# Optimization experiments

Hardware: AMD Instinct MI355X
Metric: run time of the kernel (lower is better)

## Reference

```python
import jax, jax.numpy as jnp
import numpy as np

EPS = 1e-5
SIGMA = 1.0

def _conv(x, w, stride):
    return jax.lax.conv_general_dilated(
        x, w, window_strides=(stride, stride),
        padding=[(w.shape[2] // 2, w.shape[2] // 2), (w.shape[3] // 2, w.shape[3] // 2)],
        dimension_numbers=('NCHW', 'OIHW', 'NCHW'))

def _bn(x, gamma, beta, mean, var):
    # inference-mode batchnorm over channel dim (NCHW)
    inv = gamma / jnp.sqrt(var + EPS)
    return x * inv[None, :, None, None] + (beta - mean * inv)[None, :, None, None]

def setup_inputs() -> dict:
    key = jax.random.key(0)
    ks = jax.random.split(key, 8)
    B, M, H, W, K = 8, 128, 64, 64, 6
    x = jax.random.normal(ks[0], (B, M, H, W), jnp.float32)
    cf = jax.random.normal(ks[1], (B, M, H, W), jnp.float32)
    w1 = jax.random.normal(ks[2], (M // 2, M, 3, 3), jnp.float32) * 0.05
    w2 = jax.random.normal(ks[3], (M // 4, M // 2, 3, 3), jnp.float32) * 0.05
    w3 = jax.random.normal(ks[4], (K, M // 4, 1, 1), jnp.float32) * 0.05
    def bn_params(k, c):
        k1, k2 = jax.random.split(k)
        return (jnp.ones((c,), jnp.float32),
                jnp.zeros((c,), jnp.float32),
                jax.random.normal(k1, (c,), jnp.float32) * 0.1,
                jnp.abs(jax.random.normal(k2, (c,), jnp.float32)) * 0.1 + 1.0)
    g1, b1, m1, v1 = bn_params(ks[5], M // 2)
    g2, b2, m2, v2 = bn_params(ks[6], M // 4)
    g3, b3, m3, v3 = bn_params(ks[7], K)
    return dict(x=x, center_features=cf, w1=w1, g1=g1, b1=b1, m1=m1, v1=v1,
                w2=w2, g2=g2, b2=b2, m2=m2, v2=v2,
                w3=w3, g3=g3, b3=b3, m3=m3, v3=v3)

def reference(x, center_features, w1, g1, b1, m1, v1, w2, g2, b2, m2, v2, w3, g3, b3, m3, v3):
    # center branch: conv-bn-relu x2 (stride 2) + 1x1 conv-bn, then spatial mean
    c = jax.nn.relu(_bn(_conv(center_features, w1, 2), g1, b1, m1, v1))
    c = jax.nn.relu(_bn(_conv(c, w2, 2), g2, b2, m2, v2))
    c = _bn(_conv(c, w3, 1), g3, b3, m3, v3)
    centers = c.reshape(c.shape[0], c.shape[1], -1).mean(axis=2)  # [B, K]

    B, C, H, W = x.shape
    K = centers.shape[-1]
    xf = x.reshape(B, C, H * W, 1)                      # [B,C,HW,1]
    cb = centers[:, None, None, :]                      # [B,1,1,K]
    dist = (xf - cb) ** 2                               # [B,C,HW,K]
    phi_soft = jax.nn.softmax(-SIGMA * dist, axis=-1)
    qsoft = jnp.sum(phi_soft * cb, axis=-1).reshape(B, C, H, W)
    symbols = jnp.argmin(dist, axis=-1)                 # [B,C,HW] (== argmax of hard softmax)
    qhard = centers[jnp.arange(B)[:, None, None], symbols].reshape(B, C, H, W)
    qbar = qsoft + jax.lax.stop_gradient(qhard - qsoft)
    return qbar, qsoft, qhard, symbols.reshape(B, C, H, W), centers
```

## Files before the change

### kernel.cpp

```cpp
#include <hip/hip_runtime.h>
#include <math.h>

#define BN_EPS 1e-5
#define SIGMA 1.0f

__global__ __launch_bounds__(256) void w1_to_f64_kernel(
    const float* __restrict__ w1, double* __restrict__ w1d)
{
    int i = blockIdx.x * 256 + threadIdx.x;
    if (i >= 73728) return;
    int j   = i & 7;
    int t   = i >> 3;
    int k   = t % 9;
    int t2  = t / 9;
    int ic  = t2 & 15;
    int t3  = t2 >> 4;
    int isp = t3 & 7;
    int ocg = t3 >> 3;
    w1d[i] = (double)w1[((ocg * 8 + j) * 128 + isp * 16 + ic) * 9 + k];
}

__global__ __launch_bounds__(256, 4) void conv1_partial_kernel(
    const float* __restrict__ in, const double* __restrict__ w1d,
    float* __restrict__ part)
{
    int bid = blockIdx.x;
    int oht = bid & 1;
    int b   = (bid >> 1) & 7;
    int isp = (bid >> 4) & 7;
    int ocg = bid >> 7;

    int tid = threadIdx.x;
    int ow  = tid & 31;
    int ohp = tid >> 5;
    int oh0 = oht * 16 + ohp * 2;
    int ih0 = 2 * oh0 - 1;
    int iw0 = 2 * ow - 1;

    const double* wb = w1d + (size_t)(ocg * 8 + isp) * 1152;

    double acc0[8], acc1[8];
    #pragma unroll
    for (int j = 0; j < 8; ++j) { acc0[j] = 0.0; acc1[j] = 0.0; }

    bool rowok[5], colok[3];
    #pragma unroll
    for (int t = 0; t < 5; ++t) rowok[t] = (ih0 + t) >= 0;
    #pragma unroll
    for (int t = 0; t < 3; ++t) colok[t] = (iw0 + t) >= 0;

    const float* base0 = in + ((size_t)(b * 128 + isp * 16) * 64 + ih0) * 64 + iw0;

    float cur[15];
    #pragma unroll
    for (int t = 0; t < 5; ++t)
        #pragma unroll
        for (int kw = 0; kw < 3; ++kw)
            cur[t * 3 + kw] = (rowok[t] && colok[kw]) ? base0[t * 64 + kw] : 0.f;

    for (int ic = 0; ic < 16; ++ic) {
        float nxt[15];
        if (ic + 1 < 16) {
            const float* basen = base0 + (size_t)(ic + 1) * 4096;
            #pragma unroll
            for (int t = 0; t < 5; ++t)
                #pragma unroll
                for (int kw = 0; kw < 3; ++kw)
                    nxt[t * 3 + kw] = (rowok[t] && colok[kw]) ? basen[t * 64 + kw] : 0.f;
        }
        double xv[15];
        #pragma unroll
        for (int i = 0; i < 15; ++i) xv[i] = (double)cur[i];

        const double* wk = wb + ic * 72;
        #pragma unroll
        for (int k = 0; k < 9; ++k) {
            int kh = k / 3, kw = k % 3;
            double2 wa = *(const double2*)&wk[k * 8 + 0];
            double2 wb2 = *(const double2*)&wk[k * 8 + 2];
            double2 wc = *(const double2*)&wk[k * 8 + 4];
            double2 wd = *(const double2*)&wk[k * 8 + 6];
            double x0 = xv[kh * 3 + kw];
            double x1 = xv[(kh + 2) * 3 + kw];
            acc0[0] = fma(x0, wa.x, acc0[0]);   acc1[0] = fma(x1, wa.x, acc1[0]);
            acc0[1] = fma(x0, wa.y, acc0[1]);   acc1[1] = fma(x1, wa.y, acc1[1]);
            acc0[2] = fma(x0, wb2.x, acc0[2]);  acc1[2] = fma(x1, wb2.x, acc1[2]);
            acc0[3] = fma(x0, wb2.y, acc0[3]);  acc1[3] = fma(x1, wb2.y, acc1[3]);
            acc0[4] = fma(x0, wc.x, acc0[4]);   acc1[4] = fma(x1, wc.x, acc1[4]);
            acc0[5] = fma(x0, wc.y, acc0[5]);   acc1[5] = fma(x1, wc.y, acc1[5]);
            acc0[6] = fma(x0, wd.x, acc0[6]);   acc1[6] = fma(x1, wd.x, acc1[6]);
            acc0[7] = fma(x0, wd.y, acc0[7]);   acc1[7] = fma(x1, wd.y, acc1[7]);
        }
        #pragma unroll
        for (int i = 0; i < 15; ++i) cur[i] = nxt[i];
    }

    #pragma unroll
    for (int j = 0; j < 8; ++j) {
        int idx0 = ((b * 64 + ocg * 8 + j) * 32 + oh0) * 32 + ow;
        part[isp * 524288 + idx0]      = (float)acc0[j];
        part[isp * 524288 + idx0 + 32] = (float)acc1[j];
    }
}

__global__ __launch_bounds__(256) void conv2_partial_kernel(
    const float* __restrict__ part1,
    const float* __restrict__ g1, const float* __restrict__ be1,
    const float* __restrict__ mn1, const float* __restrict__ vr1,
    const float* __restrict__ w,
    float* __restrict__ part)
{
    __shared__ float tin[4][33][36];
    __shared__ float twt[4][9][8];
    __shared__ double sinv[4], ssh[4];

    int bid = blockIdx.x;
    int ocg = bid & 3;
    int b   = (bid >> 2) & 7;
    int isp = bid >> 5;

    int tid = threadIdx.x;
    int ow  = tid & 15;
    int oh  = tid >> 4;

    if (tid < 4) {
        int ch = isp * 4 + tid;
        double inv = (double)g1[ch] / sqrt((double)vr1[ch] + BN_EPS);
        sinv[tid] = inv;
        ssh[tid]  = (double)be1[ch] - (double)mn1[ch] * inv;
    }
    __syncthreads();

    for (int lin = tid; lin < 4 * 33 * 34; lin += 256) {
        int c   = lin % 34;
        int t2  = lin / 34;
        int rr  = t2 % 33;
        int icc = t2 / 33;
        int ih  = rr - 1;
        int iw  = c - 1;
        float v = 0.f;
        if ((unsigned)ih < 32u && (unsigned)iw < 32u) {
            int ch  = isp * 4 + icc;
            int idx = ((b * 64 + ch) * 32 + ih) * 32 + iw;
            double s = 0.0;
            #pragma unroll
            for (int p = 0; p < 8; ++p) s += (double)part1[idx + p * 524288];
            double o = s * sinv[icc] + ssh[icc];
            v = fmaxf((float)o, 0.f);
        }
        tin[icc][rr][c] = v;
    }
    for (int i = tid; i < 288; i += 256) {
        int j   = i & 7;
        int k   = (i >> 3) % 9;
        int icc = i / 72;
        twt[icc][k][j] = w[(ocg * 8 + j) * 576 + (isp * 4 + icc) * 9 + k];
    }
    __syncthreads();

    double acc[8];
    #pragma unroll
    for (int j = 0; j < 8; ++j) acc[j] = 0.0;

    for (int icc = 0; icc < 4; ++icc) {
        double xv[9];
        #pragma unroll
        for (int kh = 0; kh < 3; ++kh)
            #pragma unroll
            for (int kw = 0; kw < 3; ++kw)
                xv[kh * 3 + kw] = (double)tin[icc][2 * oh + kh][2 * ow + kw];
        #pragma unroll
        for (int k = 0; k < 9; ++k) {
            float4 wa = *(const float4*)&twt[icc][k][0];
            float4 wb = *(const float4*)&twt[icc][k][4];
            acc[0] = fma(xv[k], (double)wa.x, acc[0]);
            acc[1] = fma(xv[k], (double)wa.y, acc[1]);
            acc[2] = fma(xv[k], (double)wa.z, acc[2]);
            acc[3] = fma(xv[k], (double)wa.w, acc[3]);
            acc[4] = fma(xv[k], (double)wb.x, acc[4]);
            acc[5] = fma(xv[k], (double)wb.y, acc[5]);
            acc[6] = fma(xv[k], (double)wb.z, acc[6]);
            acc[7] = fma(xv[k], (double)wb.w, acc[7]);
        }
    }
    int obase = ((b * 32 + ocg * 8) * 16 + oh) * 16 + ow;
    #pragma unroll
    for (int j = 0; j < 8; ++j)
        part[isp * 65536 + obase + j * 256] = (float)acc[j];
}

__global__ __launch_bounds__(256) void conv2_combine_ybar_kernel(
    const float* __restrict__ part,
    const float* __restrict__ g, const float* __restrict__ be,
    const float* __restrict__ mn, const float* __restrict__ vr,
    double* __restrict__ ybar)
{
    __shared__ double sm[4];
    int j  = blockIdx.x;
    int oc = j & 31;
    int t  = threadIdx.x;
    int idx = j * 256 + t;
    double s = 0.0;
    #pragma unroll
    for (int p = 0; p < 16; ++p) s += (double)part[idx + p * 65536];
    double inv = (double)g[oc] / sqrt((double)vr[oc] + BN_EPS);
    double o = s * inv + ((double)be[oc] - (double)mn[oc] * inv);
    double v = fmax(o, 0.0);
    #pragma unroll
    for (int off = 32; off > 0; off >>= 1) v += __shfl_down(v, off, 64);
    if ((t & 63) == 0) sm[t >> 6] = v;
    __syncthreads();
    if (t == 0) ybar[j] = (sm[0] + sm[1] + sm[2] + sm[3]) * (1.0 / 256.0);
}

__global__ __launch_bounds__(64) void centers_kernel(
    const double* __restrict__ ybar, const float* __restrict__ w3,
    const float* __restrict__ g, const float* __restrict__ be,
    const float* __restrict__ mn, const float* __restrict__ vr,
    double* __restrict__ cen_ws, float* __restrict__ cen_out)
{
    int t = threadIdx.x;
    if (t < 48) {
        int b = t / 6;
        int k = t % 6;
        double acc = 0.0;
        for (int ic = 0; ic < 32; ++ic) acc = fma((double)w3[k * 32 + ic], ybar[b * 32 + ic], acc);
        double inv = (double)g[k] / sqrt((double)vr[k] + BN_EPS);
        double c = acc * inv + ((double)be[k] - (double)mn[k] * inv);
        cen_ws[t]  = c;
        cen_out[t] = (float)c;
    }
}

__global__ __launch_bounds__(256) void quant_kernel(
    const float* __restrict__ x, const double* __restrict__ centers,
    float* __restrict__ qbar, float* __restrict__ qsoft,
    float* __restrict__ qhard, float* __restrict__ sym)
{
    int vid = blockIdx.x * 256 + threadIdx.x;
    int b = vid >> 17;

    double c[6];
    float cf[6];
    #pragma unroll
    for (int k = 0; k < 6; ++k) { c[k] = centers[b * 6 + k]; cf[k] = (float)c[k]; }

    float4 xv = ((const float4*)x)[vid];
    float xs[4] = {xv.x, xv.y, xv.z, xv.w};
    float r_bar[4], r_soft[4], r_hard[4], r_sym[4];

    #pragma unroll
    for (int i = 0; i < 4; ++i) {
        double xx = (double)xs[i];
        double d[6];
        double dmin = 1e300;
        int amin = 0;
        #pragma unroll
        for (int k = 0; k < 6; ++k) {
            double t = xx - c[k];
            d[k] = t * t;
            if (d[k] < dmin) { dmin = d[k]; amin = k; }
        }
        float se = 0.f, sw = 0.f;
        #pragma unroll
        for (int k = 0; k < 6; ++k) {
            float e = __expf(SIGMA * (float)(dmin - d[k]));
            se += e;
            sw += e * cf[k];
        }
        float qs = sw / se;
        float qh = cf[amin];
        r_soft[i] = qs;
        r_hard[i] = qh;
        r_bar[i]  = qh;
        r_sym[i]  = (float)amin;
    }

    ((float4*)qbar)[vid]  = make_float4(r_bar[0],  r_bar[1],  r_bar[2],  r_bar[3]);
    ((float4*)qsoft)[vid] = make_float4(r_soft[0], r_soft[1], r_soft[2], r_soft[3]);
    ((float4*)qhard)[vid] = make_float4(r_hard[0], r_hard[1], r_hard[2], r_hard[3]);
    ((float4*)sym)[vid]   = make_float4(r_sym[0],  r_sym[1],  r_sym[2],  r_sym[3]);
}

extern "C" void kernel_launch(void* const* d_in, const int* in_sizes, int n_in,
                              void* d_out, int out_size, void* d_ws, size_t ws_size,
                              hipStream_t stream) {
    const float* x  = (const float*)d_in[0];
    const float* cf = (const float*)d_in[1];
    const float* w1 = (const float*)d_in[2];
    const float* g1 = (const float*)d_in[3];
    const float* b1 = (const float*)d_in[4];
    const float* m1 = (const float*)d_in[5];
    const float* v1 = (const float*)d_in[6];
    const float* w2 = (const float*)d_in[7];
    const float* g2 = (const float*)d_in[8];
    const float* b2 = (const float*)d_in[9];
    const float* m2 = (const float*)d_in[10];
    const float* v2 = (const float*)d_in[11];
    const float* w3 = (const float*)d_in[12];
    const float* g3 = (const float*)d_in[13];
    const float* b3 = (const float*)d_in[14];
    const float* m3 = (const float*)d_in[15];
    const float* v3 = (const float*)d_in[16];

    const int NELEM = 8 * 128 * 64 * 64;
    float* out   = (float*)d_out;
    float* qbar  = out;
    float* qsoft = out + (size_t)NELEM;
    float* qhard = out + (size_t)2 * NELEM;
    float* sym   = out + (size_t)3 * NELEM;
    float* cen_o = out + (size_t)4 * NELEM;

    char* ws = (char*)d_ws;
    float*  part1 = (float*)(ws);
    float*  part2 = (float*)(ws + 16777216);
    double* yb    = (double*)(ws + 20971520);
    double* cen   = (double*)(ws + 20973568);
    double* w1d   = (double*)(ws + 20975616);

    w1_to_f64_kernel<<<288, 256, 0, stream>>>(w1, w1d);
    conv1_partial_kernel<<<1024, 256, 0, stream>>>(cf, w1d, part1);
    conv2_partial_kernel<<<512, 256, 0, stream>>>(part1, g1, b1, m1, v1, w2, part2);
    conv2_combine_ybar_kernel<<<256, 256, 0, stream>>>(part2, g2, b2, m2, v2, yb);
    centers_kernel<<<1, 64, 0, stream>>>(yb, w3, g3, b3, m3, v3, cen, cen_o);
    quant_kernel<<<NELEM / 4 / 256, 256, 0, stream>>>(x, cen, qbar, qsoft, qhard, sym);
}
```

Baseline: 188.0 us.

## Split conv1 input channels 16 ways and add separate combine+BN+ReLU kernel

Conv1's input-channel split becomes a template parameter. When the workspace is large enough it uses 16 splits, doubling the block count to 2048 for more parallelism. The partial-sum reduction, BN and ReLU move out of conv2's halo load into a dedicated vectorized combine kernel that writes y1 once. Previously each conv2 tile summed 8 partials per halo element, redundantly. The change adds an extra kernel launch and more partial-buffer traffic with 16 splits, and it drops the occupancy hint of 4 from conv1's launch bounds.

```diff
diff --git a/kernel.cpp b/kernel.cpp
--- a/kernel.cpp
+++ b/kernel.cpp
@@ -4,31 +4,35 @@
 #define BN_EPS 1e-5
 #define SIGMA 1.0f
 
+template<int NSPLIT>
 __global__ __launch_bounds__(256) void w1_to_f64_kernel(
     const float* __restrict__ w1, double* __restrict__ w1d)
 {
+    constexpr int ICN = 128 / NSPLIT;
     int i = blockIdx.x * 256 + threadIdx.x;
     if (i >= 73728) return;
     int j   = i & 7;
     int t   = i >> 3;
     int k   = t % 9;
     int t2  = t / 9;
-    int ic  = t2 & 15;
-    int t3  = t2 >> 4;
-    int isp = t3 & 7;
-    int ocg = t3 >> 3;
-    w1d[i] = (double)w1[((ocg * 8 + j) * 128 + isp * 16 + ic) * 9 + k];
-}
-
-__global__ __launch_bounds__(256, 4) void conv1_partial_kernel(
+    int ic  = t2 % ICN;
+    int t3  = t2 / ICN;
+    int isp = t3 % NSPLIT;
+    int ocg = t3 / NSPLIT;
+    w1d[i] = (double)w1[((ocg * 8 + j) * 128 + isp * ICN + ic) * 9 + k];
+}
+
+template<int NSPLIT>
+__global__ __launch_bounds__(256) void conv1_partial_kernel(
     const float* __restrict__ in, const double* __restrict__ w1d,
     float* __restrict__ part)
 {
+    constexpr int ICN = 128 / NSPLIT;
     int bid = blockIdx.x;
     int oht = bid & 1;
     int b   = (bid >> 1) & 7;
-    int isp = (bid >> 4) & 7;
-    int ocg = bid >> 7;
+    int isp = (bid >> 4) & (NSPLIT - 1);
+    int ocg = bid >> (NSPLIT == 8 ? 7 : 8);
 
     int tid = threadIdx.x;
     int ow  = tid & 31;
@@ -37,7 +41,7 @@
     int ih0 = 2 * oh0 - 1;
     int iw0 = 2 * ow - 1;
 
-    const double* wb = w1d + (size_t)(ocg * 8 + isp) * 1152;
+    const double* wb = w1d + ((size_t)ocg * NSPLIT + isp) * (ICN * 72);
 
     double acc0[8], acc1[8];
     #pragma unroll
@@ -49,7 +53,7 @@
     #pragma unroll
     for (int t = 0; t < 3; ++t) colok[t] = (iw0 + t) >= 0;
 
-    const float* base0 = in + ((size_t)(b * 128 + isp * 16) * 64 + ih0) * 64 + iw0;
+    const float* base0 = in + ((size_t)(b * 128 + isp * ICN) * 64 + ih0) * 64 + iw0;
 
     float cur[15];
     #pragma unroll
@@ -58,9 +62,9 @@
         for (int kw = 0; kw < 3; ++kw)
             cur[t * 3 + kw] = (rowok[t] && colok[kw]) ? base0[t * 64 + kw] : 0.f;
 
-    for (int ic = 0; ic < 16; ++ic) {
+    for (int ic = 0; ic < ICN; ++ic) {
         float nxt[15];
-        if (ic + 1 < 16) {
+        if (ic + 1 < ICN) {
             const float* basen = base0 + (size_t)(ic + 1) * 4096;
             #pragma unroll
             for (int t = 0; t < 5; ++t)
@@ -98,21 +102,43 @@
     #pragma unroll
     for (int j = 0; j < 8; ++j) {
         int idx0 = ((b * 64 + ocg * 8 + j) * 32 + oh0) * 32 + ow;
-        part[isp * 524288 + idx0]      = (float)acc0[j];
-        part[isp * 524288 + idx0 + 32] = (float)acc1[j];
-    }
+        part[(size_t)isp * 524288 + idx0]      = (float)acc0[j];
+        part[(size_t)isp * 524288 + idx0 + 32] = (float)acc1[j];
+    }
+}
+
+template<int NSPLIT>
+__global__ __launch_bounds__(256) void conv1_combine_kernel(
+    const float* __restrict__ part,
+    const float* __restrict__ g, const float* __restrict__ be,
+    const float* __restrict__ mn, const float* __restrict__ vr,
+    float* __restrict__ y1)
+{
+    int vid = blockIdx.x * 256 + threadIdx.x;
+    int idx = vid * 4;
+    int oc  = (idx >> 10) & 63;
+    double s0 = 0.0, s1 = 0.0, s2 = 0.0, s3 = 0.0;
+    #pragma unroll
+    for (int p = 0; p < NSPLIT; ++p) {
+        float4 v = *(const float4*)&part[idx + (size_t)p * 524288];
+        s0 += (double)v.x; s1 += (double)v.y; s2 += (double)v.z; s3 += (double)v.w;
+    }
+    double inv = (double)g[oc] / sqrt((double)vr[oc] + BN_EPS);
+    double sh  = (double)be[oc] - (double)mn[oc] * inv;
+    float4 o;
+    o.x = fmaxf((float)(s0 * inv + sh), 0.f);
+    o.y = fmaxf((float)(s1 * inv + sh), 0.f);
+    o.z = fmaxf((float)(s2 * inv + sh), 0.f);
+    o.w = fmaxf((float)(s3 * inv + sh), 0.f);
+    *(float4*)&y1[idx] = o;
 }
 
 __global__ __launch_bounds__(256) void conv2_partial_kernel(
-    const float* __restrict__ part1,
-    const float* __restrict__ g1, const float* __restrict__ be1,
-    const float* __restrict__ mn1, const float* __restrict__ vr1,
-    const float* __restrict__ w,
+    const float* __restrict__ y1, const float* __restrict__ w,
     float* __restrict__ part)
 {
     __shared__ float tin[4][33][36];
     __shared__ float twt[4][9][8];
-    __shared__ double sinv[4], ssh[4];
 
     int bid = blockIdx.x;
     int ocg = bid & 3;
@@ -123,13 +149,7 @@
     int ow  = tid & 15;
     int oh  = tid >> 4;
 
-    if (tid < 4) {
-        int ch = isp * 4 + tid;
-        double inv = (double)g1[ch] / sqrt((double)vr1[ch] + BN_EPS);
-        sinv[tid] = inv;
-        ssh[tid]  = (double)be1[ch] - (double)mn1[ch] * inv;
-    }
-    __syncthreads();
+    const float* inb = y1 + (size_t)(b * 64 + isp * 4) * 1024;
 
     for (int lin = tid; lin < 4 * 33 * 34; lin += 256) {
         int c   = lin % 34;
@@ -139,15 +159,8 @@
         int ih  = rr - 1;
         int iw  = c - 1;
         float v = 0.f;
-        if ((unsigned)ih < 32u && (unsigned)iw < 32u) {
-            int ch  = isp * 4 + icc;
-            int idx = ((b * 64 + ch) * 32 + ih) * 32 + iw;
-            double s = 0.0;
-            #pragma unroll
-            for (int p = 0; p < 8; ++p) s += (double)part1[idx + p * 524288];
-            double o = s * sinv[icc] + ssh[icc];
-            v = fmaxf((float)o, 0.f);
-        }
+        if ((unsigned)ih < 32u && (unsigned)iw < 32u)
+            v = inb[(icc * 32 + ih) * 32 + iw];
         tin[icc][rr][c] = v;
     }
     for (int i = tid; i < 288; i += 256) {
@@ -312,16 +325,41 @@
     float* cen_o = out + (size_t)4 * NELEM;
 
     char* ws = (char*)d_ws;
-    float*  part1 = (float*)(ws);
-    float*  part2 = (float*)(ws + 16777216);
-    double* yb    = (double*)(ws + 20971520);
-    double* cen   = (double*)(ws + 20973568);
-    double* w1d   = (double*)(ws + 20975616);
-
-    w1_to_f64_kernel<<<288, 256, 0, stream>>>(w1, w1d);
-    conv1_partial_kernel<<<1024, 256, 0, stream>>>(cf, w1d, part1);
-    conv2_partial_kernel<<<512, 256, 0, stream>>>(part1, g1, b1, m1, v1, w2, part2);
-    conv2_combine_ybar_kernel<<<256, 256, 0, stream>>>(part2, g2, b2, m2, v2, yb);
-    centers_kernel<<<1, 64, 0, stream>>>(yb, w3, g3, b3, m3, v3, cen, cen_o);
-    quant_kernel<<<NELEM / 4 / 256, 256, 0, stream>>>(x, cen, qbar, qsoft, qhard, sym);
-}
+    bool big = ws_size >= ((size_t)42 << 20);
+
+    if (big) {
+        const int NS = 16;
+        float*  part1 = (float*)(ws);
+        float*  y1    = (float*)(ws + (size_t)NS * 2097152);
+        float*  part2 = (float*)(ws + (size_t)NS * 2097152 + 2097152);
+        char*   tail  = ws + (size_t)NS * 2097152 + 2097152 + 4194304;
+        double* yb    = (double*)(tail);
+        double* cen   = (double*)(tail + 4096);
+        double* w1d   = (double*)(tail + 8192);
+
+        w1_to_f64_kernel<NS><<<288, 256, 0, stream>>>(w1, w1d);
+        conv1_partial_kernel<NS><<<2048, 256, 0, stream>>>(cf, w1d, part1);
+        conv1_combine_kernel<NS><<<512, 256, 0, stream>>>(part1, g1, b1, m1, v1, y1);
+        conv2_partial_kernel<<<512, 256, 0, stream>>>(y1, w2, part2);
+        conv2_combine_ybar_kernel<<<256, 256, 0, stream>>>(part2, g2, b2, m2, v2, yb);
+        centers_kernel<<<1, 64, 0, stream>>>(yb, w3, g3, b3, m3, v3, cen, cen_o);
+        quant_kernel<<<NELEM / 4 / 256, 256, 0, stream>>>(x, cen, qbar, qsoft, qhard, sym);
+    } else {
+        const int NS = 8;
+        float*  part1 = (float*)(ws);
+        float*  y1    = (float*)(ws + (size_t)NS * 2097152);
+        float*  part2 = (float*)(ws + (size_t)NS * 2097152 + 2097152);
+        char*   tail  = ws + (size_t)NS * 2097152 + 2097152 + 4194304;
+        double* yb    = (double*)(tail);
+        double* cen   = (double*)(tail + 4096);
+        double* w1d   = (double*)(tail + 8192);
+
+        w1_to_f64_kernel<NS><<<288, 256, 0, stream>>>(w1, w1d);
+        conv1_partial_kernel<NS><<<1024, 256, 0, stream>>>(cf, w1d, part1);
+        conv1_combine_kernel<NS><<<512, 256, 0, stream>>>(part1, g1, b1, m1, v1, y1);
+        conv2_partial_kernel<<<512, 256, 0, stream>>>(y1, w2, part2);
+        conv2_combine_ybar_kernel<<<256, 256, 0, stream>>>(part2, g2, b2, m2, v2, yb);
+        centers_kernel<<<1, 64, 0, stream>>>(yb, w3, g3, b3, m3, v3, cen, cen_o);
+        quant_kernel<<<NELEM / 4 / 256, 256, 0, stream>>>(x, cen, qbar, qsoft, qhard, sym);
+    }
+}
```

Result: no change. 188.4 us (+0.2%).

## Stage conv1 weights in LDS as f64, compute four output rows per thread

Applied to the files above, without the earlier changes.

Removes the separate weight-conversion kernel launch; each conv1 block now converts its slice of w1 to double directly into shared memory. Each thread computes four output rows instead of two, with 128 threads per block, so each weight load is reused across more FMAs. Input loads are restructured per kernel row, and a per-wave channel rotation staggers LDS and global access. This trades the old register prefetch of the next channel and more accumulator registers for fewer launches and more register-level reuse.

```diff
diff --git a/kernel.cpp b/kernel.cpp
--- a/kernel.cpp
+++ b/kernel.cpp
@@ -4,26 +4,12 @@
 #define BN_EPS 1e-5
 #define SIGMA 1.0f
 
-__global__ __launch_bounds__(256) void w1_to_f64_kernel(
-    const float* __restrict__ w1, double* __restrict__ w1d)
-{
-    int i = blockIdx.x * 256 + threadIdx.x;
-    if (i >= 73728) return;
-    int j   = i & 7;
-    int t   = i >> 3;
-    int k   = t % 9;
-    int t2  = t / 9;
-    int ic  = t2 & 15;
-    int t3  = t2 >> 4;
-    int isp = t3 & 7;
-    int ocg = t3 >> 3;
-    w1d[i] = (double)w1[((ocg * 8 + j) * 128 + isp * 16 + ic) * 9 + k];
-}
-
-__global__ __launch_bounds__(256, 4) void conv1_partial_kernel(
-    const float* __restrict__ in, const double* __restrict__ w1d,
+__global__ __launch_bounds__(128, 4) void conv1_partial_kernel(
+    const float* __restrict__ in, const float* __restrict__ w1,
     float* __restrict__ part)
 {
+    __shared__ double wlds[1152];
+
     int bid = blockIdx.x;
     int oht = bid & 1;
     int b   = (bid >> 1) & 7;
@@ -32,75 +18,82 @@
 
     int tid = threadIdx.x;
     int ow  = tid & 31;
-    int ohp = tid >> 5;
-    int oh0 = oht * 16 + ohp * 2;
+    int ohp = (tid >> 5) & 3;
+    int oh0 = oht * 16 + ohp * 4;
     int ih0 = 2 * oh0 - 1;
     int iw0 = 2 * ow - 1;
 
-    const double* wb = w1d + (size_t)(ocg * 8 + isp) * 1152;
-
-    double acc0[8], acc1[8];
-    #pragma unroll
-    for (int j = 0; j < 8; ++j) { acc0[j] = 0.0; acc1[j] = 0.0; }
-
-    bool rowok[5], colok[3];
-    #pragma unroll
-    for (int t = 0; t < 5; ++t) rowok[t] = (ih0 + t) >= 0;
-    #pragma unroll
-    for (int t = 0; t < 3; ++t) colok[t] = (iw0 + t) >= 0;
+    for (int i = tid; i < 1152; i += 128) {
+        int j  = i & 7;
+        int t  = i >> 3;
+        int k  = t % 9;
+        int ic = t / 9;
+        wlds[i] = (double)w1[((ocg * 8 + j) * 128 + isp * 16 + ic) * 9 + k];
+    }
+    __syncthreads();
+
+    double acc[4][8];
+    #pragma unroll
+    for (int r = 0; r < 4; ++r)
+        #pragma unroll
+        for (int j = 0; j < 8; ++j) acc[r][j] = 0.0;
+
+    bool row0ok = (ih0 >= 0);
+    bool col0ok = (iw0 >= 0);
 
     const float* base0 = in + ((size_t)(b * 128 + isp * 16) * 64 + ih0) * 64 + iw0;
 
-    float cur[15];
-    #pragma unroll
-    for (int t = 0; t < 5; ++t)
-        #pragma unroll
-        for (int kw = 0; kw < 3; ++kw)
-            cur[t * 3 + kw] = (rowok[t] && colok[kw]) ? base0[t * 64 + kw] : 0.f;
-
-    for (int ic = 0; ic < 16; ++ic) {
-        float nxt[15];
-        if (ic + 1 < 16) {
-            const float* basen = base0 + (size_t)(ic + 1) * 4096;
+    int icoff = (tid >> 6) << 3;
+
+    for (int ii = 0; ii < 16; ++ii) {
+        int ic = (ii + icoff) & 15;
+        const float* bi = base0 + (size_t)ic * 4096;
+        const double* wk = &wlds[ic * 72];
+
+        #pragma unroll
+        for (int kh = 0; kh < 3; ++kh) {
+            double xv[12];
             #pragma unroll
-            for (int t = 0; t < 5; ++t)
+            for (int r = 0; r < 4; ++r) {
+                int t = kh + 2 * r;
+                bool rok = (t > 0) || row0ok;
                 #pragma unroll
-                for (int kw = 0; kw < 3; ++kw)
-                    nxt[t * 3 + kw] = (rowok[t] && colok[kw]) ? basen[t * 64 + kw] : 0.f;
-        }
-        double xv[15];
-        #pragma unroll
-        for (int i = 0; i < 15; ++i) xv[i] = (double)cur[i];
-
-        const double* wk = wb + ic * 72;
-        #pragma unroll
-        for (int k = 0; k < 9; ++k) {
-            int kh = k / 3, kw = k % 3;
-            double2 wa = *(const double2*)&wk[k * 8 + 0];
-            double2 wb2 = *(const double2*)&wk[k * 8 + 2];
-            double2 wc = *(const double2*)&wk[k * 8 + 4];
-            double2 wd = *(const double2*)&wk[k * 8 + 6];
-            double x0 = xv[kh * 3 + kw];
-            double x1 = xv[(kh + 2) * 3 + kw];
-            acc0[0] = fma(x0, wa.x, acc0[0]);   acc1[0] = fma(x1, wa.x, acc1[0]);
-            acc0[1] = fma(x0, wa.y, acc0[1]);   acc1[1] = fma(x1, wa.y, acc1[1]);
-            acc0[2] = fma(x0, wb2.x, acc0[2]);  acc1[2] = fma(x1, wb2.x, acc1[2]);
-            acc0[3] = fma(x0, wb2.y, acc0[3]);  acc1[3] = fma(x1, wb2.y, acc1[3]);
-            acc0[4] = fma(x0, wc.x, acc0[4]);   acc1[4] = fma(x1, wc.x, acc1[4]);
-            acc0[5] = fma(x0, wc.y, acc0[5]);   acc1[5] = fma(x1, wc.y, acc1[5]);
-            acc0[6] = fma(x0, wd.x, acc0[6]);   acc1[6] = fma(x1, wd.x, acc1[6]);
-            acc0[7] = fma(x0, wd.y, acc0[7]);   acc1[7] = fma(x1, wd.y, acc1[7]);
-        }
-        #pragma unroll
-        for (int i = 0; i < 15; ++i) cur[i] = nxt[i];
-    }
-
-    #pragma unroll
-    for (int j = 0; j < 8; ++j) {
-        int idx0 = ((b * 64 + ocg * 8 + j) * 32 + oh0) * 32 + ow;
-        part[isp * 524288 + idx0]      = (float)acc0[j];
-        part[isp * 524288 + idx0 + 32] = (float)acc1[j];
-    }
+                for (int c = 0; c < 3; ++c) {
+                    bool ok = rok && ((c > 0) || col0ok);
+                    float f = ok ? bi[t * 64 + c] : 0.f;
+                    xv[r * 3 + c] = (double)f;
+                }
+            }
+            #pragma unroll
+            for (int kw = 0; kw < 3; ++kw) {
+                const double* wp = &wk[(kh * 3 + kw) * 8];
+                double2 wa = *(const double2*)&wp[0];
+                double2 wb2 = *(const double2*)&wp[2];
+                double2 wc = *(const double2*)&wp[4];
+                double2 wd = *(const double2*)&wp[6];
+                #pragma unroll
+                for (int r = 0; r < 4; ++r) {
+                    double x = xv[r * 3 + kw];
+                    acc[r][0] = fma(x, wa.x, acc[r][0]);
+                    acc[r][1] = fma(x, wa.y, acc[r][1]);
+                    acc[r][2] = fma(x, wb2.x, acc[r][2]);
+                    acc[r][3] = fma(x, wb2.y, acc[r][3]);
+                    acc[r][4] = fma(x, wc.x, acc[r][4]);
+                    acc[r][5] = fma(x, wc.y, acc[r][5]);
+                    acc[r][6] = fma(x, wd.x, acc[r][6]);
+                    acc[r][7] = fma(x, wd.y, acc[r][7]);
+                }
+            }
+        }
+    }
+
+    #pragma unroll
+    for (int r = 0; r < 4; ++r)
+        #pragma unroll
+        for (int j = 0; j < 8; ++j) {
+            int idx = ((b * 64 + ocg * 8 + j) * 32 + oh0 + r) * 32 + ow;
+            part[(size_t)isp * 524288 + idx] = (float)acc[r][j];
+        }
 }
 
 __global__ __launch_bounds__(256) void conv2_partial_kernel(
@@ -316,10 +309,8 @@
     float*  part2 = (float*)(ws + 16777216);
     double* yb    = (double*)(ws + 20971520);
     double* cen   = (double*)(ws + 20973568);
-    double* w1d   = (double*)(ws + 20975616);
-
-    w1_to_f64_kernel<<<288, 256, 0, stream>>>(w1, w1d);
-    conv1_partial_kernel<<<1024, 256, 0, stream>>>(cf, w1d, part1);
+
+    conv1_partial_kernel<<<1024, 128, 0, stream>>>(cf, w1, part1);
     conv2_partial_kernel<<<512, 256, 0, stream>>>(part1, g1, b1, m1, v1, w2, part2);
     conv2_combine_ybar_kernel<<<256, 256, 0, stream>>>(part2, g2, b2, m2, v2, yb);
     centers_kernel<<<1, 64, 0, stream>>>(yb, w3, g3, b3, m3, v3, cen, cen_o);
```

New measurement: 487.0 us. +159.1%, slower.
